# Kernel optimization log

Measured on AMD Instinct MI355X. Metric: run time of the kernel, lower is better.

Reference implementation:

```python
import jax, jax.numpy as jnp
import numpy as np
from jax import lax
import math

D_MODEL = 768
EXPAND = 2
D_INNER = EXPAND * D_MODEL          # 1536 (= d_ssm since d_ssm=None)
D_STATE = 128
HEADDIM = 64
NHEADS = D_INNER // HEADDIM         # 24
D_CONV = 4
NGROUPS = 1
CONV_DIM = D_INNER + 2 * NGROUPS * D_STATE            # 1792
D_IN_PROJ = 2 * D_INNER + 2 * NGROUPS * D_STATE + NHEADS  # d_mlp = 0
BATCH, SEQLEN = 2, 2048
EPS = 1e-5


def setup_inputs() -> dict:
    key = jax.random.key(0)
    ks = jax.random.split(key, 8)
    u = jax.random.normal(ks[0], (BATCH, SEQLEN, D_MODEL), dtype=jnp.float32)
    in_proj_w = jax.random.normal(ks[1], (D_IN_PROJ, D_MODEL), dtype=jnp.float32) / math.sqrt(D_MODEL)
    conv_w = jax.random.uniform(ks[2], (CONV_DIM, D_CONV), dtype=jnp.float32, minval=-0.5, maxval=0.5)
    conv_b = jnp.zeros((CONV_DIM,), dtype=jnp.float32)
    # dt_bias = inverse-softplus of dt sampled log-uniform in [1e-3, 1e-1]
    dt = jnp.exp(jax.random.uniform(ks[3], (NHEADS,)) * (math.log(0.1) - math.log(0.001)) + math.log(0.001))
    dt_bias = dt + jnp.log(-jnp.expm1(-dt))
    A_log = jnp.log(jax.random.uniform(ks[4], (NHEADS,), minval=1.0, maxval=16.0))
    D = jnp.ones((NHEADS,), dtype=jnp.float32)
    norm_w = jnp.ones((D_INNER,), dtype=jnp.float32)
    out_proj_w = jax.random.normal(ks[5], (D_MODEL, D_INNER), dtype=jnp.float32) / math.sqrt(D_INNER)
    return {"u": u, "in_proj_w": in_proj_w, "conv_w": conv_w, "conv_b": conv_b,
            "dt_bias": dt_bias, "A_log": A_log, "D": D, "norm_w": norm_w,
            "out_proj_w": out_proj_w}


def _mamba2_forward(u, in_proj_w, conv_w, conv_b, dt_bias, A_log, D, norm_w, out_proj_w):
    b, l, _ = u.shape
    zxbcdt = u @ in_proj_w.T                                   # [b,l,D_IN_PROJ]
    z = zxbcdt[..., :D_INNER]                                  # [b,l,d_ssm]
    xBC = zxbcdt[..., D_INNER:D_INNER + CONV_DIM]              # [b,l,conv_dim]
    dt = zxbcdt[..., D_INNER + CONV_DIM:]                      # [b,l,h]

    # causal depthwise conv1d (pad d_conv-1 left == torch pad both + truncate tail)
    xBC_t = xBC.transpose(0, 2, 1)                             # [b,c,l]
    conv_out = lax.conv_general_dilated(
        xBC_t, conv_w[:, None, :], window_strides=(1,),
        padding=[(D_CONV - 1, 0)], feature_group_count=CONV_DIM,
        dimension_numbers=("NCH", "OIH", "NCH"))
    xBC = jax.nn.silu(conv_out + conv_b[None, :, None]).transpose(0, 2, 1)  # [b,l,c]

    x = xBC[..., :D_INNER].reshape(b, l, NHEADS, HEADDIM)      # [b,l,h,p]
    B = xBC[..., D_INNER:D_INNER + D_STATE]                    # [b,l,n]
    C = xBC[..., D_INNER + D_STATE:]                           # [b,l,n]

    A = -jnp.exp(A_log)                                        # [h]
    dt_dis = jax.nn.softplus(dt + dt_bias)                     # [b,l,h]  (dt_limit=(0,inf) -> no-op clamp)
    dA = jnp.exp(dt_dis * A)                                   # [b,l,h]

    def step(state, inp):
        dA_t, dt_t, B_t, x_t, C_t = inp
        dBx = jnp.einsum("bh,bn,bhp->bhpn", dt_t, B_t, x_t)    # [b,h,p,n]
        state = lax.stop_gradient(state * dA_t[:, :, None, None] + dBx)  # matches torch .detach()
        y_t = jnp.einsum("bhpn,bn->bhp", state, C_t)
        return state, y_t

    xs = (dA.transpose(1, 0, 2), dt_dis.transpose(1, 0, 2),
          B.transpose(1, 0, 2), x.transpose(1, 0, 2, 3), C.transpose(1, 0, 2))
    state0 = jnp.zeros((b, NHEADS, HEADDIM, D_STATE), dtype=u.dtype)
    _, ys = lax.scan(step, state0, xs)                         # [l,b,h,p]
    y = ys.transpose(1, 0, 2, 3) + x * D[None, None, :, None]  # D skip (per-head)
    y = y.reshape(b, l, D_INNER)

    # gated RMSNorm (norm_before_gate=False, group_size = d_ssm)
    yz = y * jax.nn.silu(z)
    y = yz * lax.rsqrt(jnp.mean(yz * yz, axis=-1, keepdims=True) + EPS) * norm_w

    return y @ out_proj_w.T                                    # [b,l,d_model]


def reference(u, in_proj_w, conv_w, conv_b, dt_bias, A_log, D, norm_w, out_proj_w):
    return _mamba2_forward(u, in_proj_w, conv_w, conv_b, dt_bias, A_log, D, norm_w, out_proj_w)
```

## Files before the change

### kernel.cpp

```cpp
#include <hip/hip_runtime.h>
#include <hip/hip_bf16.h>
#include <math.h>

#define D_MODEL   768
#define D_INNER   1536
#define D_STATE   128
#define HEADDIM   64
#define NHEADS    24
#define D_CONV    4
#define CONV_DIM  1792
#define D_IN_PROJ 3352
#define BATCH     2
#define SEQLEN    2048
#define NROWS     (BATCH*SEQLEN)
#define EPS       1e-5f

#define NCHUNK    16
#define CHUNK     128
#define STATE_SZ  (HEADDIM*D_STATE)

#define N1_PAD    3456
#define LDST      136
#define H72       72

typedef __bf16 bf16x8 __attribute__((ext_vector_type(8)));
typedef float  f32x4  __attribute__((ext_vector_type(4)));
typedef short  s16x8  __attribute__((ext_vector_type(8)));

__device__ __forceinline__ short f2b(float f) {
    unsigned u = __float_as_uint(f);
    unsigned r = (u + 0x7FFFu + ((u >> 16) & 1u)) >> 16;
    return (short)r;
}
__device__ __forceinline__ float b2f(short s) {
    return __uint_as_float(((unsigned)(unsigned short)s) << 16);
}

template<typename OT>
__global__ __launch_bounds__(256) void gemm_bf16_kernel(
    const short* __restrict__ A, const short* __restrict__ W,
    OT* __restrict__ C, int K, int Nreal)
{
    __shared__ short smem[2][2][128][32];
    const int m0 = blockIdx.y * 128;
    const int n0 = blockIdx.x * 128;
    const int tid  = threadIdx.x;
    const int lane = tid & 63;
    const int wid  = tid >> 6;
    const int wm = wid >> 1, wn = wid & 1;
    const int lr = lane & 15;
    const int kg = lane >> 4;

    f32x4 acc[4][4];
    #pragma unroll
    for (int i = 0; i < 4; ++i)
        #pragma unroll
        for (int j = 0; j < 4; ++j)
            acc[i][j] = (f32x4){0.f, 0.f, 0.f, 0.f};

    const int srow = (lane >> 2);
    const int scol = (lane & 3) * 8;

    auto STAGE = [&](int buf, int k0) {
        #pragma unroll
        for (int it = 0; it < 2; ++it) {
            int r = wid * 32 + it * 16;
            const short* ga = A + (size_t)(m0 + r + srow) * K + k0 + scol;
            const short* gw = W + (size_t)(n0 + r + srow) * K + k0 + scol;
            __builtin_amdgcn_global_load_lds(
                (const __attribute__((address_space(1))) void*)ga,
                (__attribute__((address_space(3))) void*)&smem[buf][0][r][0], 16, 0, 0);
            __builtin_amdgcn_global_load_lds(
                (const __attribute__((address_space(1))) void*)gw,
                (__attribute__((address_space(3))) void*)&smem[buf][1][r][0], 16, 0, 0);
        }
    };
    auto COMPUTE = [&](int buf) {
        bf16x8 af[4], bf[4];
        #pragma unroll
        for (int i = 0; i < 4; ++i)
            af[i] = *(const bf16x8*)&smem[buf][0][wm * 64 + i * 16 + lr][kg * 8];
        #pragma unroll
        for (int j = 0; j < 4; ++j)
            bf[j] = *(const bf16x8*)&smem[buf][1][wn * 64 + j * 16 + lr][kg * 8];
        #pragma unroll
        for (int i = 0; i < 4; ++i)
            #pragma unroll
            for (int j = 0; j < 4; ++j)
                acc[i][j] = __builtin_amdgcn_mfma_f32_16x16x32_bf16(af[i], bf[j], acc[i][j], 0, 0, 0);
    };

    const int nt = K >> 5;
    STAGE(0, 0);
    __syncthreads();
    int cur = 0;
    for (int t = 0; t < nt - 1; ++t) {
        STAGE(cur ^ 1, (t + 1) << 5);
        COMPUTE(cur);
        __syncthreads();
        cur ^= 1;
    }
    COMPUTE(cur);

    if constexpr (sizeof(OT) == 2) {
        __syncthreads();
        short* eb = &smem[0][0][0][0];
        #pragma unroll
        for (int i = 0; i < 4; ++i) {
            #pragma unroll
            for (int j = 0; j < 4; ++j) {
                #pragma unroll
                for (int r = 0; r < 4; ++r) {
                    int row = wm * 64 + i * 16 + kg * 4 + r;
                    int col = wn * 64 + j * 16 + lr;
                    eb[row * 128 + col] = f2b(acc[i][j][r]);
                }
            }
        }
        __syncthreads();
        #pragma unroll
        for (int ch = 0; ch < 8; ++ch) {
            int cidx = ch * 256 + tid;
            int row  = cidx >> 4;
            int cp   = cidx & 15;
            int ncol = n0 + cp * 8;
            if (ncol < Nreal)
                *(s16x8*)((short*)C + (size_t)(m0 + row) * Nreal + ncol) =
                    *(const s16x8*)(eb + row * 128 + cp * 8);
        }
    } else {
        #pragma unroll
        for (int i = 0; i < 4; ++i) {
            int mrow = m0 + wm * 64 + i * 16 + kg * 4;
            #pragma unroll
            for (int j = 0; j < 4; ++j) {
                int ncol = n0 + wn * 64 + j * 16 + lr;
                if (ncol < Nreal) {
                    #pragma unroll
                    for (int r = 0; r < 4; ++r)
                        C[(size_t)(mrow + r) * Nreal + ncol] = acc[i][j][r];
                }
            }
        }
    }
}

__global__ __launch_bounds__(256) void cast_bf16_kernel(
    const float* __restrict__ in, short* __restrict__ out, int n4)
{
    int i = blockIdx.x * 256 + threadIdx.x;
    if (i >= n4) return;
    float4 v = *(const float4*)(in + (size_t)i * 4);
    short4 o = make_short4(f2b(v.x), f2b(v.y), f2b(v.z), f2b(v.w));
    *(short4*)(out + (size_t)i * 4) = o;
}

__global__ __launch_bounds__(256) void cast_pad_w1_kernel(
    const float* __restrict__ w, short* __restrict__ wb)
{
    int i = blockIdx.x * 256 + threadIdx.x;
    const int n4 = N1_PAD * D_MODEL / 4;
    if (i >= n4) return;
    size_t base = (size_t)i * 4;
    int row = (int)(base / D_MODEL);
    float4 v = make_float4(0.f, 0.f, 0.f, 0.f);
    if (row < D_IN_PROJ) v = *(const float4*)(w + base);
    short4 o = make_short4(f2b(v.x), f2b(v.y), f2b(v.z), f2b(v.w));
    *(short4*)(wb + base) = o;
}

__global__ __launch_bounds__(256) void conv_silu_kernel(
    const short* __restrict__ zxb, short* __restrict__ cob,
    const float* __restrict__ cw, const float* __restrict__ cb)
{
    const int NG = CONV_DIM / 8;
    int idx = blockIdx.x * 256 + threadIdx.x;
    int g = idx % NG;
    int r = idx / NG;
    int c0 = g * 8;
    int l = r & (SEQLEN - 1);

    float4 w[8];
    #pragma unroll
    for (int e = 0; e < 8; ++e)
        w[e] = *(const float4*)(cw + (size_t)(c0 + e) * 4);

    float acc[8];
    #pragma unroll
    for (int e = 0; e < 8; ++e) acc[e] = cb[c0 + e];

    #pragma unroll
    for (int tap = 0; tap < 4; ++tap) {
        if (l - 3 + tap >= 0) {
            s16x8 v = *(const s16x8*)(zxb + (size_t)(r - 3 + tap) * D_IN_PROJ + D_INNER + c0);
            #pragma unroll
            for (int e = 0; e < 8; ++e) {
                float we = (tap == 0) ? w[e].x : (tap == 1) ? w[e].y : (tap == 2) ? w[e].z : w[e].w;
                acc[e] = fmaf(b2f(v[e]), we, acc[e]);
            }
        }
    }
    s16x8 o;
    #pragma unroll
    for (int e = 0; e < 8; ++e)
        o[e] = f2b(acc[e] / (1.f + expf(-acc[e])));
    *(s16x8*)(cob + (size_t)r * CONV_DIM + c0) = o;
}

__global__ __launch_bounds__(256) void dt_kernel(
    const short* __restrict__ zxb, const float* __restrict__ dt_bias,
    const float* __restrict__ A_log, float* __restrict__ dtb, float* __restrict__ dta)
{
    int idx = blockIdx.x * 256 + threadIdx.x;
    if (idx >= NROWS * NHEADS) return;
    int r = idx / NHEADS, h = idx - r * NHEADS;
    float x = b2f(zxb[(size_t)r * D_IN_PROJ + (D_INNER + CONV_DIM) + h]) + dt_bias[h];
    float sp = (x > 20.f) ? x : log1pf(expf(x));
    float A  = -expf(A_log[h]);
    dtb[idx] = sp;
    dta[idx] = sp * A;
}

__global__ __launch_bounds__(512) void ssd_intra(
    const short* __restrict__ co, const float* __restrict__ dtb,
    const float* __restrict__ dta, const float* __restrict__ Dvec,
    float* __restrict__ ybuf, float* __restrict__ sstate, float* __restrict__ cumW)
{
    __shared__ short lds[26112];
    __shared__ float clg[128];
    __shared__ float dts[128];

    int t = blockIdx.x;
    int c = t & 15;
    int hb = t >> 4;
    int h = hb % NHEADS;
    int b = hb / NHEADS;
    const int R0 = b * SEQLEN + c * CHUNK;
    const int tid  = threadIdx.x;
    const int lane = tid & 63;
    const int wid  = tid >> 6;
    const int lr = lane & 15;
    const int kg = lane >> 4;
    const short* cobase = co + (size_t)R0 * CONV_DIM;

    if (tid < 128) {
        clg[tid] = dta[(size_t)(R0 + tid) * NHEADS + h];
        dts[tid] = dtb[(size_t)(R0 + tid) * NHEADS + h];
    }
    __syncthreads();
    for (int off = 1; off < 128; off <<= 1) {
        float v = 0.f;
        if (tid < 128 && tid >= off) v = clg[tid - off];
        __syncthreads();
        if (tid < 128) clg[tid] += v;
        __syncthreads();
    }
    const float clgE = clg[127];
    if (tid < 128)
        cumW[((size_t)(b * NHEADS + h)) * SEQLEN + c * CHUNK + tid] = __expf(clg[tid]);

    short* CsH = lds;
    short* BsH = lds + 128 * H72;
    const int wmS = wid >> 2, wnS = wid & 3;
    f32x4 accS[4][2];
    #pragma unroll
    for (int i = 0; i < 4; ++i)
        #pragma unroll
        for (int j = 0; j < 2; ++j)
            accS[i][j] = (f32x4){0.f, 0.f, 0.f, 0.f};

    for (int kh = 0; kh < 2; ++kh) {
        {
            int r = tid >> 2, q = tid & 3;
            const short* cr = cobase + (size_t)r * CONV_DIM + (D_INNER + D_STATE) + kh * 64 + q * 16;
            const short* br = cobase + (size_t)r * CONV_DIM + D_INNER + kh * 64 + q * 16;
            *(s16x8*)(CsH + r * H72 + q * 16)     = *(const s16x8*)cr;
            *(s16x8*)(CsH + r * H72 + q * 16 + 8) = *(const s16x8*)(cr + 8);
            *(s16x8*)(BsH + r * H72 + q * 16)     = *(const s16x8*)br;
            *(s16x8*)(BsH + r * H72 + q * 16 + 8) = *(const s16x8*)(br + 8);
        }
        __syncthreads();
        #pragma unroll
        for (int kk = 0; kk < 2; ++kk) {
            bf16x8 af[4], bf[2];
            #pragma unroll
            for (int i = 0; i < 4; ++i)
                af[i] = *(const bf16x8*)(CsH + (wmS * 64 + i * 16 + lr) * H72 + kk * 32 + kg * 8);
            #pragma unroll
            for (int j = 0; j < 2; ++j)
                bf[j] = *(const bf16x8*)(BsH + (wnS * 32 + j * 16 + lr) * H72 + kk * 32 + kg * 8);
            #pragma unroll
            for (int i = 0; i < 4; ++i)
                #pragma unroll
                for (int j = 0; j < 2; ++j)
                    accS[i][j] = __builtin_amdgcn_mfma_f32_16x16x32_bf16(af[i], bf[j], accS[i][j], 0, 0, 0);
        }
        __syncthreads();
    }

    short* Ps = lds;
    short* Xt = lds + 128 * LDST;
    #pragma unroll
    for (int i = 0; i < 4; ++i) {
        #pragma unroll
        for (int j = 0; j < 2; ++j) {
            #pragma unroll
            for (int r = 0; r < 4; ++r) {
                int l  = wmS * 64 + i * 16 + kg * 4 + r;
                int lp = wnS * 32 + j * 16 + lr;
                float w = (lp <= l) ? __expf(clg[l] - clg[lp]) : 0.f;
                Ps[l * LDST + lp] = f2b(accS[i][j][r] * w);
            }
        }
    }
    if (tid < 256) {
        int r = tid >> 1, q = tid & 1;
        const short* xr = cobase + (size_t)r * CONV_DIM + h * HEADDIM + q * 32;
        float dtv = dts[r];
        #pragma unroll
        for (int i = 0; i < 4; ++i) {
            s16x8 xv = *(const s16x8*)(xr + i * 8);
            #pragma unroll
            for (int e = 0; e < 8; ++e) {
                int p = q * 32 + i * 8 + e;
                Xt[p * LDST + r] = f2b(b2f(xv[e]) * dtv);
            }
        }
    }
    __syncthreads();

    {
        int wm = wid >> 1, wn = wid & 1;
        f32x4 acc[2][2];
        #pragma unroll
        for (int i = 0; i < 2; ++i)
            #pragma unroll
            for (int j = 0; j < 2; ++j)
                acc[i][j] = (f32x4){0.f, 0.f, 0.f, 0.f};
        #pragma unroll
        for (int kk = 0; kk < 4; ++kk) {
            bf16x8 af[2], bf[2];
            #pragma unroll
            for (int i = 0; i < 2; ++i)
                af[i] = *(const bf16x8*)(Ps + (wm * 32 + i * 16 + lr) * LDST + kk * 32 + kg * 8);
            #pragma unroll
            for (int j = 0; j < 2; ++j)
                bf[j] = *(const bf16x8*)(Xt + (wn * 32 + j * 16 + lr) * LDST + kk * 32 + kg * 8);
            #pragma unroll
            for (int i = 0; i < 2; ++i)
                #pragma unroll
                for (int j = 0; j < 2; ++j)
                    acc[i][j] = __builtin_amdgcn_mfma_f32_16x16x32_bf16(af[i], bf[j], acc[i][j], 0, 0, 0);
        }
        const float Dh = Dvec[h];
        #pragma unroll
        for (int i = 0; i < 2; ++i) {
            #pragma unroll
            for (int j = 0; j < 2; ++j) {
                #pragma unroll
                for (int r = 0; r < 4; ++r) {
                    int l = wm * 32 + i * 16 + kg * 4 + r;
                    int p = wn * 32 + j * 16 + lr;
                    float xval = b2f(cobase[(size_t)l * CONV_DIM + h * HEADDIM + p]);
                    ybuf[(size_t)(R0 + l) * D_INNER + h * HEADDIM + p] = acc[i][j][r] + Dh * xval;
                }
            }
        }
    }
    __syncthreads();

    short* Bt = lds;
    {
        int r = tid >> 2, q = tid & 3;
        const short* br = cobase + (size_t)r * CONV_DIM + D_INNER + q * 32;
        float wstr = __expf(clgE - clg[r]);
        #pragma unroll
        for (int i = 0; i < 4; ++i) {
            s16x8 bv = *(const s16x8*)(br + i * 8);
            #pragma unroll
            for (int e = 0; e < 8; ++e) {
                int n = q * 32 + i * 8 + e;
                Bt[n * LDST + r] = f2b(b2f(bv[e]) * wstr);
            }
        }
    }
    __syncthreads();

    {
        int wm = wid >> 2, wn = wid & 3;
        f32x4 acc[2][2];
        #pragma unroll
        for (int i = 0; i < 2; ++i)
            #pragma unroll
            for (int j = 0; j < 2; ++j)
                acc[i][j] = (f32x4){0.f, 0.f, 0.f, 0.f};
        #pragma unroll
        for (int kk = 0; kk < 4; ++kk) {
            bf16x8 af[2], bf[2];
            #pragma unroll
            for (int i = 0; i < 2; ++i)
                af[i] = *(const bf16x8*)(Xt + (wm * 32 + i * 16 + lr) * LDST + kk * 32 + kg * 8);
            #pragma unroll
            for (int j = 0; j < 2; ++j)
                bf[j] = *(const bf16x8*)(Bt + (wn * 32 + j * 16 + lr) * LDST + kk * 32 + kg * 8);
            #pragma unroll
            for (int i = 0; i < 2; ++i)
                #pragma unroll
                for (int j = 0; j < 2; ++j)
                    acc[i][j] = __builtin_amdgcn_mfma_f32_16x16x32_bf16(af[i], bf[j], acc[i][j], 0, 0, 0);
        }
        float* sbase = sstate + (((size_t)(b * NHEADS + h)) * NCHUNK + c) * STATE_SZ;
        #pragma unroll
        for (int i = 0; i < 2; ++i) {
            #pragma unroll
            for (int j = 0; j < 2; ++j) {
                #pragma unroll
                for (int r = 0; r < 4; ++r) {
                    int p = wm * 32 + i * 16 + kg * 4 + r;
                    int n = wn * 32 + j * 16 + lr;
                    sbase[p * D_STATE + n] = acc[i][j][r];
                }
            }
        }
    }
}

__global__ __launch_bounds__(128) void scan_chunk_prefix(
    const float* __restrict__ cumW, float* __restrict__ sstate)
{
    int blk = blockIdx.x;
    int piece = blk & 15;
    int bh = blk >> 4;
    int tid = threadIdx.x;
    float* base = sstate + (size_t)bh * NCHUNK * STATE_SZ + piece * 512 + tid * 4;
    const float* cw = cumW + (size_t)bh * SEQLEN;
    float4 run = make_float4(0.f, 0.f, 0.f, 0.f);
    for (int c = 0; c < NCHUNK; ++c) {
        float Ac = cw[c * CHUNK + (CHUNK - 1)];
        float* ptr = base + (size_t)c * STATE_SZ;
        float4 loc = *(float4*)ptr;
        *(float4*)ptr = run;
        run.x = fmaf(Ac, run.x, loc.x);
        run.y = fmaf(Ac, run.y, loc.y);
        run.z = fmaf(Ac, run.z, loc.z);
        run.w = fmaf(Ac, run.w, loc.w);
    }
}

__global__ __launch_bounds__(256) void ssd_inter(
    const short* __restrict__ co, const float* __restrict__ cumW,
    const float* __restrict__ sstate, float* __restrict__ ybuf)
{
    __shared__ short lds[26112];
    short* Cs = lds;
    short* Sn = lds + 128 * LDST;

    int t = blockIdx.x;
    int c = t & 15;
    int hb = t >> 4;
    int h = hb % NHEADS;
    int b = hb / NHEADS;
    const int R0 = b * SEQLEN + c * CHUNK;
    const int tid  = threadIdx.x;
    const int lane = tid & 63;
    const int wid  = tid >> 6;
    const int lr = lane & 15;
    const int kg = lane >> 4;
    const short* cobase = co + (size_t)R0 * CONV_DIM;

    {
        int r = tid >> 1, q = tid & 1;
        const short* cr = cobase + (size_t)r * CONV_DIM + (D_INNER + D_STATE) + q * 64;
        #pragma unroll
        for (int i = 0; i < 8; ++i)
            *(s16x8*)(Cs + r * LDST + q * 64 + i * 8) = *(const s16x8*)(cr + i * 8);
    }
    {
        int r = tid >> 2, q = tid & 3;
        const float* sr = sstate + (((size_t)(b * NHEADS + h)) * NCHUNK + c) * STATE_SZ
                          + (size_t)r * D_STATE + q * 32;
        #pragma unroll
        for (int i = 0; i < 8; ++i) {
            float4 sv = *(const float4*)(sr + i * 4);
            *(short4*)(Sn + r * LDST + q * 32 + i * 4) =
                make_short4(f2b(sv.x), f2b(sv.y), f2b(sv.z), f2b(sv.w));
        }
    }
    __syncthreads();

    int wm = wid >> 1, wn = wid & 1;
    f32x4 acc[4][2];
    #pragma unroll
    for (int i = 0; i < 4; ++i)
        #pragma unroll
        for (int j = 0; j < 2; ++j)
            acc[i][j] = (f32x4){0.f, 0.f, 0.f, 0.f};
    #pragma unroll
    for (int kk = 0; kk < 4; ++kk) {
        bf16x8 af[4], bf[2];
        #pragma unroll
        for (int i = 0; i < 4; ++i)
            af[i] = *(const bf16x8*)(Cs + (wm * 64 + i * 16 + lr) * LDST + kk * 32 + kg * 8);
        #pragma unroll
        for (int j = 0; j < 2; ++j)
            bf[j] = *(const bf16x8*)(Sn + (wn * 32 + j * 16 + lr) * LDST + kk * 32 + kg * 8);
        #pragma unroll
        for (int i = 0; i < 4; ++i)
            #pragma unroll
            for (int j = 0; j < 2; ++j)
                acc[i][j] = __builtin_amdgcn_mfma_f32_16x16x32_bf16(af[i], bf[j], acc[i][j], 0, 0, 0);
    }
    const float* cwrow = cumW + ((size_t)(b * NHEADS + h)) * SEQLEN + c * CHUNK;
    #pragma unroll
    for (int i = 0; i < 4; ++i) {
        #pragma unroll
        for (int j = 0; j < 2; ++j) {
            #pragma unroll
            for (int r = 0; r < 4; ++r) {
                int l = wm * 64 + i * 16 + kg * 4 + r;
                int p = wn * 32 + j * 16 + lr;
                float w = cwrow[l];
                size_t idx = (size_t)(R0 + l) * D_INNER + h * HEADDIM + p;
                ybuf[idx] += w * acc[i][j][r];
            }
        }
    }
}

__global__ __launch_bounds__(256) void gate_norm_kernel(
    const short* __restrict__ zxb, const float* __restrict__ ybuf,
    const float* __restrict__ norm_w, short* __restrict__ yn)
{
    int r = blockIdx.x;
    const short* zrow = zxb + (size_t)r * D_IN_PROJ;
    const float* yrow = ybuf + (size_t)r * D_INNER;
    float vals[6];
    float ss = 0.f;
    #pragma unroll
    for (int i = 0; i < 6; ++i) {
        int c = threadIdx.x + i * 256;
        float z = b2f(zrow[c]);
        float y = yrow[c];
        float v = y * (z / (1.f + expf(-z)));
        vals[i] = v;
        ss = fmaf(v, v, ss);
    }
    ss += __shfl_xor(ss, 1);
    ss += __shfl_xor(ss, 2);
    ss += __shfl_xor(ss, 4);
    ss += __shfl_xor(ss, 8);
    ss += __shfl_xor(ss, 16);
    ss += __shfl_xor(ss, 32);
    __shared__ float red[4];
    if ((threadIdx.x & 63) == 0) red[threadIdx.x >> 6] = ss;
    __syncthreads();
    float tot = red[0] + red[1] + red[2] + red[3];
    float scale = rsqrtf(tot / (float)D_INNER + EPS);
    #pragma unroll
    for (int i = 0; i < 6; ++i) {
        int c = threadIdx.x + i * 256;
        yn[(size_t)r * D_INNER + c] = f2b(vals[i] * scale * norm_w[c]);
    }
}

extern "C" void kernel_launch(void* const* d_in, const int* in_sizes, int n_in,
                              void* d_out, int out_size, void* d_ws, size_t ws_size,
                              hipStream_t stream) {
    const float* u          = (const float*)d_in[0];
    const float* in_proj_w  = (const float*)d_in[1];
    const float* conv_w     = (const float*)d_in[2];
    const float* conv_b     = (const float*)d_in[3];
    const float* dt_bias    = (const float*)d_in[4];
    const float* A_log      = (const float*)d_in[5];
    const float* Dvec       = (const float*)d_in[6];
    const float* norm_w     = (const float*)d_in[7];
    const float* out_proj_w = (const float*)d_in[8];
    float* out = (float*)d_out;

    short* zxb    = (short*)d_ws;
    short* cob    = zxb + (size_t)NROWS * D_IN_PROJ;
    float* dtb    = (float*)(cob + (size_t)NROWS * CONV_DIM);
    float* dta    = dtb  + (size_t)NROWS * NHEADS;
    float* ybuf   = dta  + (size_t)NROWS * NHEADS;
    float* sstate = ybuf + (size_t)NROWS * D_INNER;
    float* cumW   = sstate + (size_t)BATCH*NHEADS*NCHUNK*STATE_SZ;

    short* ub  = (short*)ybuf;
    short* w1b = ub + (size_t)NROWS * D_MODEL;
    short* ynb = (short*)sstate;
    short* w2b = zxb;

    cast_bf16_kernel<<<(NROWS*D_MODEL/4 + 255)/256, 256, 0, stream>>>(u, ub, NROWS*D_MODEL/4);
    cast_pad_w1_kernel<<<(N1_PAD*D_MODEL/4 + 255)/256, 256, 0, stream>>>(in_proj_w, w1b);
    gemm_bf16_kernel<short><<<dim3(N1_PAD/128, NROWS/128), 256, 0, stream>>>(ub, w1b, zxb, D_MODEL, D_IN_PROJ);
    conv_silu_kernel<<<NROWS*(CONV_DIM/8)/256, 256, 0, stream>>>(zxb, cob, conv_w, conv_b);
    dt_kernel<<<(NROWS*NHEADS + 255)/256, 256, 0, stream>>>(zxb, dt_bias, A_log, dtb, dta);
    ssd_intra<<<BATCH*NHEADS*NCHUNK, 512, 0, stream>>>(cob, dtb, dta, Dvec, ybuf, sstate, cumW);
    scan_chunk_prefix<<<BATCH*NHEADS*16, 128, 0, stream>>>(cumW, sstate);
    ssd_inter<<<BATCH*NHEADS*NCHUNK, 256, 0, stream>>>(cob, cumW, sstate, ybuf);
    gate_norm_kernel<<<NROWS, 256, 0, stream>>>(zxb, ybuf, norm_w, ynb);
    cast_bf16_kernel<<<(D_MODEL*D_INNER/4 + 255)/256, 256, 0, stream>>>(out_proj_w, w2b, D_MODEL*D_INNER/4);
    gemm_bf16_kernel<float><<<dim3(D_MODEL/128, NROWS/128), 256, 0, stream>>>(ynb, w2b, out, D_INNER, D_MODEL);
}
```

Before: 243.3 us.

## Restructure SSD kernels, fuse y output in bf16, swizzle GEMM grids, add N64 out-proj GEMM

Splits the SSD work into a state-only kernel and a single y kernel that computes the intra-chunk diagonal term, the inter-chunk state contribution and the D skip together. The y kernel writes bf16 through LDS instead of a float read-modify-write, which removes one full pass over the y buffer. Separately, both GEMMs get a swizzled 1D grid for L2 locality, the output projection uses a new 128x64 tile kernel to launch more blocks, and gate_norm is vectorized with 192 threads. The costs are extra LDS staging in the y kernel and bf16 rounding of y before the norm.

```diff
diff --git a/kernel.cpp b/kernel.cpp
--- a/kernel.cpp
+++ b/kernel.cpp
@@ -36,14 +36,15 @@
     return __uint_as_float(((unsigned)(unsigned short)s) << 16);
 }
 
-template<typename OT>
 __global__ __launch_bounds__(256) void gemm_bf16_kernel(
     const short* __restrict__ A, const short* __restrict__ W,
-    OT* __restrict__ C, int K, int Nreal)
+    short* __restrict__ C, int K, int Nreal, int NT)
 {
     __shared__ short smem[2][2][128][32];
-    const int m0 = blockIdx.y * 128;
-    const int n0 = blockIdx.x * 128;
+    int flat = blockIdx.x;
+    int swz  = (flat & 7) * (gridDim.x >> 3) + (flat >> 3);
+    const int m0 = (swz / NT) * 128;
+    const int n0 = (swz % NT) * 128;
     const int tid  = threadIdx.x;
     const int lane = tid & 63;
     const int wid  = tid >> 6;
@@ -102,45 +103,108 @@
     }
     COMPUTE(cur);
 
-    if constexpr (sizeof(OT) == 2) {
+    __syncthreads();
+    short* eb = &smem[0][0][0][0];
+    #pragma unroll
+    for (int i = 0; i < 4; ++i)
+        #pragma unroll
+        for (int j = 0; j < 4; ++j)
+            #pragma unroll
+            for (int r = 0; r < 4; ++r) {
+                int row = wm * 64 + i * 16 + kg * 4 + r;
+                int col = wn * 64 + j * 16 + lr;
+                eb[row * 128 + col] = f2b(acc[i][j][r]);
+            }
+    __syncthreads();
+    #pragma unroll
+    for (int ch = 0; ch < 8; ++ch) {
+        int cidx = ch * 256 + tid;
+        int row  = cidx >> 4;
+        int cp   = cidx & 15;
+        int ncol = n0 + cp * 8;
+        if (ncol < Nreal)
+            *(s16x8*)(C + (size_t)(m0 + row) * Nreal + ncol) =
+                *(const s16x8*)(eb + row * 128 + cp * 8);
+    }
+}
+
+__global__ __launch_bounds__(256) void gemm_bf16_n64_kernel(
+    const short* __restrict__ A, const short* __restrict__ W,
+    float* __restrict__ C, int K, int N, int NT)
+{
+    __shared__ short As[2][128][32];
+    __shared__ short Ws[2][64][32];
+    int flat = blockIdx.x;
+    int swz  = (flat & 7) * (gridDim.x >> 3) + (flat >> 3);
+    const int m0 = (swz / NT) * 128;
+    const int n0 = (swz % NT) * 64;
+    const int tid  = threadIdx.x;
+    const int lane = tid & 63;
+    const int wid  = tid >> 6;
+    const int lr = lane & 15;
+    const int kg = lane >> 4;
+
+    f32x4 acc[2][4];
+    #pragma unroll
+    for (int i = 0; i < 2; ++i)
+        #pragma unroll
+        for (int j = 0; j < 4; ++j)
+            acc[i][j] = (f32x4){0.f, 0.f, 0.f, 0.f};
+
+    const int srow = (lane >> 2);
+    const int scol = (lane & 3) * 8;
+
+    auto STAGE = [&](int buf, int k0) {
+        #pragma unroll
+        for (int it = 0; it < 2; ++it) {
+            int r = wid * 32 + it * 16;
+            const short* ga = A + (size_t)(m0 + r + srow) * K + k0 + scol;
+            __builtin_amdgcn_global_load_lds(
+                (const __attribute__((address_space(1))) void*)ga,
+                (__attribute__((address_space(3))) void*)&As[buf][r][0], 16, 0, 0);
+        }
+        int r2 = wid * 16;
+        const short* gw = W + (size_t)(n0 + r2 + srow) * K + k0 + scol;
+        __builtin_amdgcn_global_load_lds(
+            (const __attribute__((address_space(1))) void*)gw,
+            (__attribute__((address_space(3))) void*)&Ws[buf][r2][0], 16, 0, 0);
+    };
+    auto COMPUTE = [&](int buf) {
+        bf16x8 af[2], bf[4];
+        #pragma unroll
+        for (int i = 0; i < 2; ++i)
+            af[i] = *(const bf16x8*)&As[buf][wid * 32 + i * 16 + lr][kg * 8];
+        #pragma unroll
+        for (int j = 0; j < 4; ++j)
+            bf[j] = *(const bf16x8*)&Ws[buf][j * 16 + lr][kg * 8];
+        #pragma unroll
+        for (int i = 0; i < 2; ++i)
+            #pragma unroll
+            for (int j = 0; j < 4; ++j)
+                acc[i][j] = __builtin_amdgcn_mfma_f32_16x16x32_bf16(af[i], bf[j], acc[i][j], 0, 0, 0);
+    };
+
+    const int nt = K >> 5;
+    STAGE(0, 0);
+    __syncthreads();
+    int cur = 0;
+    for (int t = 0; t < nt - 1; ++t) {
+        STAGE(cur ^ 1, (t + 1) << 5);
+        COMPUTE(cur);
         __syncthreads();
-        short* eb = &smem[0][0][0][0];
-        #pragma unroll
-        for (int i = 0; i < 4; ++i) {
-            #pragma unroll
-            for (int j = 0; j < 4; ++j) {
-                #pragma unroll
-                for (int r = 0; r < 4; ++r) {
-                    int row = wm * 64 + i * 16 + kg * 4 + r;
-                    int col = wn * 64 + j * 16 + lr;
-                    eb[row * 128 + col] = f2b(acc[i][j][r]);
-                }
-            }
-        }
-        __syncthreads();
-        #pragma unroll
-        for (int ch = 0; ch < 8; ++ch) {
-            int cidx = ch * 256 + tid;
-            int row  = cidx >> 4;
-            int cp   = cidx & 15;
-            int ncol = n0 + cp * 8;
-            if (ncol < Nreal)
-                *(s16x8*)((short*)C + (size_t)(m0 + row) * Nreal + ncol) =
-                    *(const s16x8*)(eb + row * 128 + cp * 8);
-        }
-    } else {
-        #pragma unroll
-        for (int i = 0; i < 4; ++i) {
-            int mrow = m0 + wm * 64 + i * 16 + kg * 4;
-            #pragma unroll
-            for (int j = 0; j < 4; ++j) {
-                int ncol = n0 + wn * 64 + j * 16 + lr;
-                if (ncol < Nreal) {
-                    #pragma unroll
-                    for (int r = 0; r < 4; ++r)
-                        C[(size_t)(mrow + r) * Nreal + ncol] = acc[i][j][r];
-                }
-            }
+        cur ^= 1;
+    }
+    COMPUTE(cur);
+
+    #pragma unroll
+    for (int i = 0; i < 2; ++i) {
+        int mrow = m0 + wid * 32 + i * 16 + kg * 4;
+        #pragma unroll
+        for (int j = 0; j < 4; ++j) {
+            int ncol = n0 + j * 16 + lr;
+            #pragma unroll
+            for (int r = 0; r < 4; ++r)
+                C[(size_t)(mrow + r) * N + ncol] = acc[i][j][r];
         }
     }
 }
@@ -221,10 +285,10 @@
     dta[idx] = sp * A;
 }
 
-__global__ __launch_bounds__(512) void ssd_intra(
+__global__ __launch_bounds__(256) void ssd_states(
     const short* __restrict__ co, const float* __restrict__ dtb,
-    const float* __restrict__ dta, const float* __restrict__ Dvec,
-    float* __restrict__ ybuf, float* __restrict__ sstate, float* __restrict__ cumW)
+    const float* __restrict__ dta, float* __restrict__ sstate,
+    float* __restrict__ cumW, float* __restrict__ clgbuf)
 {
     __shared__ short lds[26112];
     __shared__ float clg[128];
@@ -256,173 +320,69 @@
         __syncthreads();
     }
     const float clgE = clg[127];
-    if (tid < 128)
-        cumW[((size_t)(b * NHEADS + h)) * SEQLEN + c * CHUNK + tid] = __expf(clg[tid]);
-
-    short* CsH = lds;
-    short* BsH = lds + 128 * H72;
-    const int wmS = wid >> 2, wnS = wid & 3;
-    f32x4 accS[4][2];
-    #pragma unroll
-    for (int i = 0; i < 4; ++i)
-        #pragma unroll
-        for (int j = 0; j < 2; ++j)
-            accS[i][j] = (f32x4){0.f, 0.f, 0.f, 0.f};
-
-    for (int kh = 0; kh < 2; ++kh) {
-        {
-            int r = tid >> 2, q = tid & 3;
-            const short* cr = cobase + (size_t)r * CONV_DIM + (D_INNER + D_STATE) + kh * 64 + q * 16;
-            const short* br = cobase + (size_t)r * CONV_DIM + D_INNER + kh * 64 + q * 16;
-            *(s16x8*)(CsH + r * H72 + q * 16)     = *(const s16x8*)cr;
-            *(s16x8*)(CsH + r * H72 + q * 16 + 8) = *(const s16x8*)(cr + 8);
-            *(s16x8*)(BsH + r * H72 + q * 16)     = *(const s16x8*)br;
-            *(s16x8*)(BsH + r * H72 + q * 16 + 8) = *(const s16x8*)(br + 8);
-        }
-        __syncthreads();
-        #pragma unroll
-        for (int kk = 0; kk < 2; ++kk) {
-            bf16x8 af[4], bf[2];
-            #pragma unroll
-            for (int i = 0; i < 4; ++i)
-                af[i] = *(const bf16x8*)(CsH + (wmS * 64 + i * 16 + lr) * H72 + kk * 32 + kg * 8);
-            #pragma unroll
-            for (int j = 0; j < 2; ++j)
-                bf[j] = *(const bf16x8*)(BsH + (wnS * 32 + j * 16 + lr) * H72 + kk * 32 + kg * 8);
-            #pragma unroll
-            for (int i = 0; i < 4; ++i)
-                #pragma unroll
-                for (int j = 0; j < 2; ++j)
-                    accS[i][j] = __builtin_amdgcn_mfma_f32_16x16x32_bf16(af[i], bf[j], accS[i][j], 0, 0, 0);
-        }
-        __syncthreads();
-    }
-
-    short* Ps = lds;
+    if (tid < 128) {
+        size_t o = ((size_t)(b * NHEADS + h)) * SEQLEN + c * CHUNK + tid;
+        cumW[o]   = __expf(clg[tid]);
+        clgbuf[o] = clg[tid];
+    }
+
+    short* Bt = lds;
     short* Xt = lds + 128 * LDST;
-    #pragma unroll
-    for (int i = 0; i < 4; ++i) {
-        #pragma unroll
-        for (int j = 0; j < 2; ++j) {
-            #pragma unroll
-            for (int r = 0; r < 4; ++r) {
-                int l  = wmS * 64 + i * 16 + kg * 4 + r;
-                int lp = wnS * 32 + j * 16 + lr;
-                float w = (lp <= l) ? __expf(clg[l] - clg[lp]) : 0.f;
-                Ps[l * LDST + lp] = f2b(accS[i][j][r] * w);
-            }
-        }
-    }
-    if (tid < 256) {
+    {
         int r = tid >> 1, q = tid & 1;
+        float dtv = dts[r];
         const short* xr = cobase + (size_t)r * CONV_DIM + h * HEADDIM + q * 32;
-        float dtv = dts[r];
         #pragma unroll
         for (int i = 0; i < 4; ++i) {
             s16x8 xv = *(const s16x8*)(xr + i * 8);
             #pragma unroll
-            for (int e = 0; e < 8; ++e) {
-                int p = q * 32 + i * 8 + e;
-                Xt[p * LDST + r] = f2b(b2f(xv[e]) * dtv);
+            for (int e = 0; e < 8; ++e)
+                Xt[(q * 32 + i * 8 + e) * LDST + r] = f2b(b2f(xv[e]) * dtv);
+        }
+        float wstr = __expf(clgE - clg[r]);
+        const short* br = cobase + (size_t)r * CONV_DIM + D_INNER + q * 64;
+        #pragma unroll
+        for (int i = 0; i < 8; ++i) {
+            s16x8 bv = *(const s16x8*)(br + i * 8);
+            #pragma unroll
+            for (int e = 0; e < 8; ++e)
+                Bt[(q * 64 + i * 8 + e) * LDST + r] = f2b(b2f(bv[e]) * wstr);
+        }
+    }
+    __syncthreads();
+
+    f32x4 acc[4][2];
+    #pragma unroll
+    for (int i = 0; i < 4; ++i)
+        #pragma unroll
+        for (int j = 0; j < 2; ++j)
+            acc[i][j] = (f32x4){0.f, 0.f, 0.f, 0.f};
+    #pragma unroll
+    for (int kk = 0; kk < 4; ++kk) {
+        bf16x8 af[4], bf[2];
+        #pragma unroll
+        for (int i = 0; i < 4; ++i)
+            af[i] = *(const bf16x8*)(Xt + (i * 16 + lr) * LDST + kk * 32 + kg * 8);
+        #pragma unroll
+        for (int j = 0; j < 2; ++j)
+            bf[j] = *(const bf16x8*)(Bt + (wid * 32 + j * 16 + lr) * LDST + kk * 32 + kg * 8);
+        #pragma unroll
+        for (int i = 0; i < 4; ++i)
+            #pragma unroll
+            for (int j = 0; j < 2; ++j)
+                acc[i][j] = __builtin_amdgcn_mfma_f32_16x16x32_bf16(af[i], bf[j], acc[i][j], 0, 0, 0);
+    }
+    float* sbase = sstate + (((size_t)(b * NHEADS + h)) * NCHUNK + c) * STATE_SZ;
+    #pragma unroll
+    for (int i = 0; i < 4; ++i)
+        #pragma unroll
+        for (int j = 0; j < 2; ++j)
+            #pragma unroll
+            for (int r = 0; r < 4; ++r) {
+                int p = i * 16 + kg * 4 + r;
+                int n = wid * 32 + j * 16 + lr;
+                sbase[p * D_STATE + n] = acc[i][j][r];
             }
-        }
-    }
-    __syncthreads();
-
-    {
-        int wm = wid >> 1, wn = wid & 1;
-        f32x4 acc[2][2];
-        #pragma unroll
-        for (int i = 0; i < 2; ++i)
-            #pragma unroll
-            for (int j = 0; j < 2; ++j)
-                acc[i][j] = (f32x4){0.f, 0.f, 0.f, 0.f};
-        #pragma unroll
-        for (int kk = 0; kk < 4; ++kk) {
-            bf16x8 af[2], bf[2];
-            #pragma unroll
-            for (int i = 0; i < 2; ++i)
-                af[i] = *(const bf16x8*)(Ps + (wm * 32 + i * 16 + lr) * LDST + kk * 32 + kg * 8);
-            #pragma unroll
-            for (int j = 0; j < 2; ++j)
-                bf[j] = *(const bf16x8*)(Xt + (wn * 32 + j * 16 + lr) * LDST + kk * 32 + kg * 8);
-            #pragma unroll
-            for (int i = 0; i < 2; ++i)
-                #pragma unroll
-                for (int j = 0; j < 2; ++j)
-                    acc[i][j] = __builtin_amdgcn_mfma_f32_16x16x32_bf16(af[i], bf[j], acc[i][j], 0, 0, 0);
-        }
-        const float Dh = Dvec[h];
-        #pragma unroll
-        for (int i = 0; i < 2; ++i) {
-            #pragma unroll
-            for (int j = 0; j < 2; ++j) {
-                #pragma unroll
-                for (int r = 0; r < 4; ++r) {
-                    int l = wm * 32 + i * 16 + kg * 4 + r;
-                    int p = wn * 32 + j * 16 + lr;
-                    float xval = b2f(cobase[(size_t)l * CONV_DIM + h * HEADDIM + p]);
-                    ybuf[(size_t)(R0 + l) * D_INNER + h * HEADDIM + p] = acc[i][j][r] + Dh * xval;
-                }
-            }
-        }
-    }
-    __syncthreads();
-
-    short* Bt = lds;
-    {
-        int r = tid >> 2, q = tid & 3;
-        const short* br = cobase + (size_t)r * CONV_DIM + D_INNER + q * 32;
-        float wstr = __expf(clgE - clg[r]);
-        #pragma unroll
-        for (int i = 0; i < 4; ++i) {
-            s16x8 bv = *(const s16x8*)(br + i * 8);
-            #pragma unroll
-            for (int e = 0; e < 8; ++e) {
-                int n = q * 32 + i * 8 + e;
-                Bt[n * LDST + r] = f2b(b2f(bv[e]) * wstr);
-            }
-        }
-    }
-    __syncthreads();
-
-    {
-        int wm = wid >> 2, wn = wid & 3;
-        f32x4 acc[2][2];
-        #pragma unroll
-        for (int i = 0; i < 2; ++i)
-            #pragma unroll
-            for (int j = 0; j < 2; ++j)
-                acc[i][j] = (f32x4){0.f, 0.f, 0.f, 0.f};
-        #pragma unroll
-        for (int kk = 0; kk < 4; ++kk) {
-            bf16x8 af[2], bf[2];
-            #pragma unroll
-            for (int i = 0; i < 2; ++i)
-                af[i] = *(const bf16x8*)(Xt + (wm * 32 + i * 16 + lr) * LDST + kk * 32 + kg * 8);
-            #pragma unroll
-            for (int j = 0; j < 2; ++j)
-                bf[j] = *(const bf16x8*)(Bt + (wn * 32 + j * 16 + lr) * LDST + kk * 32 + kg * 8);
-            #pragma unroll
-            for (int i = 0; i < 2; ++i)
-                #pragma unroll
-                for (int j = 0; j < 2; ++j)
-                    acc[i][j] = __builtin_amdgcn_mfma_f32_16x16x32_bf16(af[i], bf[j], acc[i][j], 0, 0, 0);
-        }
-        float* sbase = sstate + (((size_t)(b * NHEADS + h)) * NCHUNK + c) * STATE_SZ;
-        #pragma unroll
-        for (int i = 0; i < 2; ++i) {
-            #pragma unroll
-            for (int j = 0; j < 2; ++j) {
-                #pragma unroll
-                for (int r = 0; r < 4; ++r) {
-                    int p = wm * 32 + i * 16 + kg * 4 + r;
-                    int n = wn * 32 + j * 16 + lr;
-                    sbase[p * D_STATE + n] = acc[i][j][r];
-                }
-            }
-        }
-    }
 }
 
 __global__ __launch_bounds__(128) void scan_chunk_prefix(
@@ -447,13 +407,14 @@
     }
 }
 
-__global__ __launch_bounds__(256) void ssd_inter(
-    const short* __restrict__ co, const float* __restrict__ cumW,
-    const float* __restrict__ sstate, float* __restrict__ ybuf)
+__global__ __launch_bounds__(512) void ssd_y(
+    const short* __restrict__ co, const float* __restrict__ dtb,
+    const float* __restrict__ clgbuf, const float* __restrict__ sstate,
+    const float* __restrict__ Dvec, short* __restrict__ ybuf)
 {
     __shared__ short lds[26112];
-    short* Cs = lds;
-    short* Sn = lds + 128 * LDST;
+    __shared__ float clg[128];
+    __shared__ float dts[128];
 
     int t = blockIdx.x;
     int c = t & 15;
@@ -468,81 +429,189 @@
     const int kg = lane >> 4;
     const short* cobase = co + (size_t)R0 * CONV_DIM;
 
-    {
+    if (tid < 128) {
+        size_t o = ((size_t)(b * NHEADS + h)) * SEQLEN + c * CHUNK + tid;
+        clg[tid] = clgbuf[o];
+        dts[tid] = dtb[(size_t)(R0 + tid) * NHEADS + h];
+    }
+    __syncthreads();
+
+    short* CsH = lds;
+    short* BsH = lds + 128 * H72;
+    const int wmS = wid >> 2, wnS = wid & 3;
+    f32x4 accS[4][2];
+    #pragma unroll
+    for (int i = 0; i < 4; ++i)
+        #pragma unroll
+        for (int j = 0; j < 2; ++j)
+            accS[i][j] = (f32x4){0.f, 0.f, 0.f, 0.f};
+
+    for (int kh = 0; kh < 2; ++kh) {
+        {
+            int r = tid >> 2, q = tid & 3;
+            const short* cr = cobase + (size_t)r * CONV_DIM + (D_INNER + D_STATE) + kh * 64 + q * 16;
+            const short* br = cobase + (size_t)r * CONV_DIM + D_INNER + kh * 64 + q * 16;
+            *(s16x8*)(CsH + r * H72 + q * 16)     = *(const s16x8*)cr;
+            *(s16x8*)(CsH + r * H72 + q * 16 + 8) = *(const s16x8*)(cr + 8);
+            *(s16x8*)(BsH + r * H72 + q * 16)     = *(const s16x8*)br;
+            *(s16x8*)(BsH + r * H72 + q * 16 + 8) = *(const s16x8*)(br + 8);
+        }
+        __syncthreads();
+        #pragma unroll
+        for (int kk = 0; kk < 2; ++kk) {
+            bf16x8 af[4], bf[2];
+            #pragma unroll
+            for (int i = 0; i < 4; ++i)
+                af[i] = *(const bf16x8*)(CsH + (wmS * 64 + i * 16 + lr) * H72 + kk * 32 + kg * 8);
+            #pragma unroll
+            for (int j = 0; j < 2; ++j)
+                bf[j] = *(const bf16x8*)(BsH + (wnS * 32 + j * 16 + lr) * H72 + kk * 32 + kg * 8);
+            #pragma unroll
+            for (int i = 0; i < 4; ++i)
+                #pragma unroll
+                for (int j = 0; j < 2; ++j)
+                    accS[i][j] = __builtin_amdgcn_mfma_f32_16x16x32_bf16(af[i], bf[j], accS[i][j], 0, 0, 0);
+        }
+        __syncthreads();
+    }
+
+    short* Ps = lds;
+    short* Xt = lds + 128 * LDST;
+    #pragma unroll
+    for (int i = 0; i < 4; ++i)
+        #pragma unroll
+        for (int j = 0; j < 2; ++j)
+            #pragma unroll
+            for (int r = 0; r < 4; ++r) {
+                int l  = wmS * 64 + i * 16 + kg * 4 + r;
+                int lp = wnS * 32 + j * 16 + lr;
+                float w = (lp <= l) ? __expf(clg[l] - clg[lp]) : 0.f;
+                Ps[l * LDST + lp] = f2b(accS[i][j][r] * w);
+            }
+    if (tid < 256) {
         int r = tid >> 1, q = tid & 1;
-        const short* cr = cobase + (size_t)r * CONV_DIM + (D_INNER + D_STATE) + q * 64;
-        #pragma unroll
-        for (int i = 0; i < 8; ++i)
-            *(s16x8*)(Cs + r * LDST + q * 64 + i * 8) = *(const s16x8*)(cr + i * 8);
-    }
+        const short* xr = cobase + (size_t)r * CONV_DIM + h * HEADDIM + q * 32;
+        float dtv = dts[r];
+        #pragma unroll
+        for (int i = 0; i < 4; ++i) {
+            s16x8 xv = *(const s16x8*)(xr + i * 8);
+            #pragma unroll
+            for (int e = 0; e < 8; ++e)
+                Xt[(q * 32 + i * 8 + e) * LDST + r] = f2b(b2f(xv[e]) * dtv);
+        }
+    }
+    __syncthreads();
+
+    const int wm = wid >> 1, wn = wid & 1;
+    f32x4 acc1[2][2];
+    #pragma unroll
+    for (int i = 0; i < 2; ++i)
+        #pragma unroll
+        for (int j = 0; j < 2; ++j)
+            acc1[i][j] = (f32x4){0.f, 0.f, 0.f, 0.f};
+    #pragma unroll
+    for (int kk = 0; kk < 4; ++kk) {
+        bf16x8 af[2], bf[2];
+        #pragma unroll
+        for (int i = 0; i < 2; ++i)
+            af[i] = *(const bf16x8*)(Ps + (wm * 32 + i * 16 + lr) * LDST + kk * 32 + kg * 8);
+        #pragma unroll
+        for (int j = 0; j < 2; ++j)
+            bf[j] = *(const bf16x8*)(Xt + (wn * 32 + j * 16 + lr) * LDST + kk * 32 + kg * 8);
+        #pragma unroll
+        for (int i = 0; i < 2; ++i)
+            #pragma unroll
+            for (int j = 0; j < 2; ++j)
+                acc1[i][j] = __builtin_amdgcn_mfma_f32_16x16x32_bf16(af[i], bf[j], acc1[i][j], 0, 0, 0);
+    }
+    __syncthreads();
+
+    short* Cs = lds;
+    short* Sn = lds + 128 * LDST;
     {
         int r = tid >> 2, q = tid & 3;
+        const short* cr = cobase + (size_t)r * CONV_DIM + (D_INNER + D_STATE) + q * 32;
+        #pragma unroll
+        for (int i = 0; i < 4; ++i)
+            *(s16x8*)(Cs + r * LDST + q * 32 + i * 8) = *(const s16x8*)(cr + i * 8);
+    }
+    {
+        int r = tid >> 3, q = tid & 7;
         const float* sr = sstate + (((size_t)(b * NHEADS + h)) * NCHUNK + c) * STATE_SZ
-                          + (size_t)r * D_STATE + q * 32;
-        #pragma unroll
-        for (int i = 0; i < 8; ++i) {
+                          + (size_t)r * D_STATE + q * 16;
+        #pragma unroll
+        for (int i = 0; i < 4; ++i) {
             float4 sv = *(const float4*)(sr + i * 4);
-            *(short4*)(Sn + r * LDST + q * 32 + i * 4) =
+            *(short4*)(Sn + r * LDST + q * 16 + i * 4) =
                 make_short4(f2b(sv.x), f2b(sv.y), f2b(sv.z), f2b(sv.w));
         }
     }
     __syncthreads();
 
-    int wm = wid >> 1, wn = wid & 1;
-    f32x4 acc[4][2];
-    #pragma unroll
-    for (int i = 0; i < 4; ++i)
-        #pragma unroll
-        for (int j = 0; j < 2; ++j)
-            acc[i][j] = (f32x4){0.f, 0.f, 0.f, 0.f};
+    f32x4 acc2[2][2];
+    #pragma unroll
+    for (int i = 0; i < 2; ++i)
+        #pragma unroll
+        for (int j = 0; j < 2; ++j)
+            acc2[i][j] = (f32x4){0.f, 0.f, 0.f, 0.f};
     #pragma unroll
     for (int kk = 0; kk < 4; ++kk) {
-        bf16x8 af[4], bf[2];
-        #pragma unroll
-        for (int i = 0; i < 4; ++i)
-            af[i] = *(const bf16x8*)(Cs + (wm * 64 + i * 16 + lr) * LDST + kk * 32 + kg * 8);
+        bf16x8 af[2], bf[2];
+        #pragma unroll
+        for (int i = 0; i < 2; ++i)
+            af[i] = *(const bf16x8*)(Cs + (wm * 32 + i * 16 + lr) * LDST + kk * 32 + kg * 8);
         #pragma unroll
         for (int j = 0; j < 2; ++j)
             bf[j] = *(const bf16x8*)(Sn + (wn * 32 + j * 16 + lr) * LDST + kk * 32 + kg * 8);
         #pragma unroll
-        for (int i = 0; i < 4; ++i)
+        for (int i = 0; i < 2; ++i)
             #pragma unroll
             for (int j = 0; j < 2; ++j)
-                acc[i][j] = __builtin_amdgcn_mfma_f32_16x16x32_bf16(af[i], bf[j], acc[i][j], 0, 0, 0);
-    }
-    const float* cwrow = cumW + ((size_t)(b * NHEADS + h)) * SEQLEN + c * CHUNK;
-    #pragma unroll
-    for (int i = 0; i < 4; ++i) {
-        #pragma unroll
-        for (int j = 0; j < 2; ++j) {
+                acc2[i][j] = __builtin_amdgcn_mfma_f32_16x16x32_bf16(af[i], bf[j], acc2[i][j], 0, 0, 0);
+    }
+    __syncthreads();
+
+    short* yt = lds;
+    const float Dh = Dvec[h];
+    #pragma unroll
+    for (int i = 0; i < 2; ++i)
+        #pragma unroll
+        for (int j = 0; j < 2; ++j)
             #pragma unroll
             for (int r = 0; r < 4; ++r) {
-                int l = wm * 64 + i * 16 + kg * 4 + r;
+                int l = wm * 32 + i * 16 + kg * 4 + r;
                 int p = wn * 32 + j * 16 + lr;
-                float w = cwrow[l];
-                size_t idx = (size_t)(R0 + l) * D_INNER + h * HEADDIM + p;
-                ybuf[idx] += w * acc[i][j][r];
+                float cw = __expf(clg[l]);
+                float xval = b2f(cobase[(size_t)l * CONV_DIM + h * HEADDIM + p]);
+                yt[l * H72 + p] = f2b(acc1[i][j][r] + cw * acc2[i][j][r] + Dh * xval);
             }
-        }
-    }
-}
-
-__global__ __launch_bounds__(256) void gate_norm_kernel(
-    const short* __restrict__ zxb, const float* __restrict__ ybuf,
+    __syncthreads();
+    #pragma unroll
+    for (int k = 0; k < 2; ++k) {
+        int idx = tid * 2 + k;
+        int row = idx >> 3;
+        int cp  = idx & 7;
+        *(s16x8*)(ybuf + (size_t)(R0 + row) * D_INNER + h * HEADDIM + cp * 8) =
+            *(const s16x8*)(yt + row * H72 + cp * 8);
+    }
+}
+
+__global__ __launch_bounds__(192) void gate_norm_kernel(
+    const short* __restrict__ zxb, const short* __restrict__ ybuf,
     const float* __restrict__ norm_w, short* __restrict__ yn)
 {
     int r = blockIdx.x;
-    const short* zrow = zxb + (size_t)r * D_IN_PROJ;
-    const float* yrow = ybuf + (size_t)r * D_INNER;
-    float vals[6];
+    int c0 = threadIdx.x * 8;
+    s16x8 zv = *(const s16x8*)(zxb + (size_t)r * D_IN_PROJ + c0);
+    s16x8 yv = *(const s16x8*)(ybuf + (size_t)r * D_INNER + c0);
+    float vals[8];
     float ss = 0.f;
     #pragma unroll
-    for (int i = 0; i < 6; ++i) {
-        int c = threadIdx.x + i * 256;
-        float z = b2f(zrow[c]);
-        float y = yrow[c];
+    for (int e = 0; e < 8; ++e) {
+        float z = b2f(zv[e]);
+        float y = b2f(yv[e]);
         float v = y * (z / (1.f + expf(-z)));
-        vals[i] = v;
+        vals[e] = v;
         ss = fmaf(v, v, ss);
     }
     ss += __shfl_xor(ss, 1);
@@ -551,16 +620,19 @@
     ss += __shfl_xor(ss, 8);
     ss += __shfl_xor(ss, 16);
     ss += __shfl_xor(ss, 32);
-    __shared__ float red[4];
+    __shared__ float red[3];
     if ((threadIdx.x & 63) == 0) red[threadIdx.x >> 6] = ss;
     __syncthreads();
-    float tot = red[0] + red[1] + red[2] + red[3];
+    float tot = red[0] + red[1] + red[2];
     float scale = rsqrtf(tot / (float)D_INNER + EPS);
-    #pragma unroll
-    for (int i = 0; i < 6; ++i) {
-        int c = threadIdx.x + i * 256;
-        yn[(size_t)r * D_INNER + c] = f2b(vals[i] * scale * norm_w[c]);
-    }
+    float4 nw0 = *(const float4*)(norm_w + c0);
+    float4 nw1 = *(const float4*)(norm_w + c0 + 4);
+    const float nw[8] = {nw0.x, nw0.y, nw0.z, nw0.w, nw1.x, nw1.y, nw1.z, nw1.w};
+    s16x8 o;
+    #pragma unroll
+    for (int e = 0; e < 8; ++e)
+        o[e] = f2b(vals[e] * scale * nw[e]);
+    *(s16x8*)(yn + (size_t)r * D_INNER + c0) = o;
 }
 
 extern "C" void kernel_launch(void* const* d_in, const int* in_sizes, int n_in,
@@ -581,24 +653,25 @@
     short* cob    = zxb + (size_t)NROWS * D_IN_PROJ;
     float* dtb    = (float*)(cob + (size_t)NROWS * CONV_DIM);
     float* dta    = dtb  + (size_t)NROWS * NHEADS;
-    float* ybuf   = dta  + (size_t)NROWS * NHEADS;
-    float* sstate = ybuf + (size_t)NROWS * D_INNER;
+    short* ybuf   = (short*)(dta + (size_t)NROWS * NHEADS);
+    float* sstate = (float*)(ybuf + (size_t)NROWS * D_INNER);
     float* cumW   = sstate + (size_t)BATCH*NHEADS*NCHUNK*STATE_SZ;
-
-    short* ub  = (short*)ybuf;
+    float* clgbuf = cumW + (size_t)BATCH*NHEADS*SEQLEN;
+
+    short* ub  = (short*)sstate;
     short* w1b = ub + (size_t)NROWS * D_MODEL;
     short* ynb = (short*)sstate;
     short* w2b = zxb;
 
     cast_bf16_kernel<<<(NROWS*D_MODEL/4 + 255)/256, 256, 0, stream>>>(u, ub, NROWS*D_MODEL/4);
     cast_pad_w1_kernel<<<(N1_PAD*D_MODEL/4 + 255)/256, 256, 0, stream>>>(in_proj_w, w1b);
-    gemm_bf16_kernel<short><<<dim3(N1_PAD/128, NROWS/128), 256, 0, stream>>>(ub, w1b, zxb, D_MODEL, D_IN_PROJ);
+    gemm_bf16_kernel<<<(NROWS/128)*(N1_PAD/128), 256, 0, stream>>>(ub, w1b, zxb, D_MODEL, D_IN_PROJ, N1_PAD/128);
     conv_silu_kernel<<<NROWS*(CONV_DIM/8)/256, 256, 0, stream>>>(zxb, cob, conv_w, conv_b);
     dt_kernel<<<(NROWS*NHEADS + 255)/256, 256, 0, stream>>>(zxb, dt_bias, A_log, dtb, dta);
-    ssd_intra<<<BATCH*NHEADS*NCHUNK, 512, 0, stream>>>(cob, dtb, dta, Dvec, ybuf, sstate, cumW);
+    ssd_states<<<BATCH*NHEADS*NCHUNK, 256, 0, stream>>>(cob, dtb, dta, sstate, cumW, clgbuf);
     scan_chunk_prefix<<<BATCH*NHEADS*16, 128, 0, stream>>>(cumW, sstate);
-    ssd_inter<<<BATCH*NHEADS*NCHUNK, 256, 0, stream>>>(cob, cumW, sstate, ybuf);
-    gate_norm_kernel<<<NROWS, 256, 0, stream>>>(zxb, ybuf, norm_w, ynb);
+    ssd_y<<<BATCH*NHEADS*NCHUNK, 512, 0, stream>>>(cob, dtb, clgbuf, sstate, Dvec, ybuf);
+    gate_norm_kernel<<<NROWS, 192, 0, stream>>>(zxb, ybuf, norm_w, ynb);
     cast_bf16_kernel<<<(D_MODEL*D_INNER/4 + 255)/256, 256, 0, stream>>>(out_proj_w, w2b, D_MODEL*D_INNER/4);
-    gemm_bf16_kernel<float><<<dim3(D_MODEL/128, NROWS/128), 256, 0, stream>>>(ynb, w2b, out, D_INNER, D_MODEL);
-}
+    gemm_bf16_n64_kernel<<<(NROWS/128)*(D_MODEL/64), 256, 0, stream>>>(ynb, w2b, out, D_INNER, D_MODEL, D_MODEL/64);
+}
```

Result: faster. 236.0 us (-3.0%).
